# Performance work log

Measured on AMD Instinct MI355X. Metric: run time of the kernel, lower is better.

The kernel has to match this reference:

```python
import jax, jax.numpy as jnp
import numpy as np

N0 = 100000; E0 = 1600000; N1 = 100000; E1 = 1600000; G = 512
F0 = 93; F1 = 43
BN_EPS = 1e-5


def setup_inputs() -> dict:
    key = jax.random.key(0)
    ks = jax.random.split(key, 20)
    p = lambda i, shape: jax.random.normal(ks[i], shape, jnp.float32) * 0.02
    return {
        "x_0": jax.random.normal(ks[0], (N0, F0), jnp.float32),
        "x_1": jax.random.normal(ks[1], (N1, F1), jnp.float32),
        "edge_index_0": jax.random.randint(ks[2], (2, E0), 0, N0, jnp.int32),
        "edge_index_1": jax.random.randint(ks[3], (2, E1), 0, N1, jnp.int32),
        "batch_0": jnp.sort(jax.random.randint(ks[4], (N0,), 0, G, jnp.int32)),
        "batch_1": jnp.sort(jax.random.randint(ks[5], (N1,), 0, G, jnp.int32)),
        "w_c1": p(6, (F0, F0)), "b_c1": jnp.zeros((F0,), jnp.float32),
        "w_c2": p(7, (F0, F0 * 10)), "b_c2": jnp.zeros((F0 * 10,), jnp.float32),
        "w_c3": p(8, (F1, F1)), "b_c3": jnp.zeros((F1,), jnp.float32),
        "w_c4": p(9, (F1, F1 * 10)), "b_c4": jnp.zeros((F1 * 10,), jnp.float32),
        "g0_w1": p(10, (F0 * 10 * 2, 1024)), "g0_b1": jnp.zeros((1024,), jnp.float32),
        "g0_w2": p(11, (1024, 512)), "g0_b2": jnp.zeros((512,), jnp.float32),
        "g0_bn_g": jnp.ones((512,), jnp.float32), "g0_bn_b": jnp.zeros((512,), jnp.float32),
        "g1_w1": p(12, (F1 * 10 * 2, 1024)), "g1_b1": jnp.zeros((1024,), jnp.float32),
        "g1_w2": p(13, (1024, 512)), "g1_b2": jnp.zeros((512,), jnp.float32),
        "g1_bn_g": jnp.ones((512,), jnp.float32), "g1_bn_b": jnp.zeros((512,), jnp.float32),
        "f0_w1": p(14, (512, 256)), "f0_b1": jnp.zeros((256,), jnp.float32),
        "f0_w2": p(15, (256, 2)), "f0_b2": jnp.zeros((2,), jnp.float32),
        "f1_w1": p(16, (512, 256)), "f1_b1": jnp.zeros((256,), jnp.float32),
        "f1_w2": p(17, (256, 2)), "f1_b2": jnp.zeros((2,), jnp.float32),
    }


def gin_conv(x, edge_index, W, b):
    # GINConv(eps=0): nn(x + sum_{j->i} x_j); messages from src=edge_index[0] to dst=edge_index[1]
    agg = jax.ops.segment_sum(x[edge_index[0]], edge_index[1], num_segments=x.shape[0])
    return (x + agg) @ W + b


def pool_mean_max(x, batch):
    cnt = jax.ops.segment_sum(jnp.ones((x.shape[0], 1), x.dtype), batch, num_segments=G)
    mean = jax.ops.segment_sum(x, batch, num_segments=G) / jnp.maximum(cnt, 1.0)
    mx = jax.ops.segment_max(x, batch, num_segments=G)
    mx = jnp.where(cnt > 0, mx, 0.0)
    return jnp.concatenate([mean, mx], axis=1)


def batchnorm(x, g, b):
    m = x.mean(axis=0)
    v = x.var(axis=0)
    return g * (x - m) / jnp.sqrt(v + BN_EPS) + b


def branch(x, ei, batch, w_a, b_a, w_b, b_b, w1, b1, w2, b2, bn_g, bn_b):
    h = jax.nn.relu(gin_conv(x, ei, w_a, b_a))
    h = jax.nn.relu(gin_conv(h, ei, w_b, b_b))
    h = pool_mean_max(h, batch)              # [G, 2*10*F] ; PairNorm(mode='None') is identity
    h = jax.nn.relu(h @ w1 + b1)             # dropout: eval mode (identity)
    h = h @ w2 + b2
    return batchnorm(h, bn_g, bn_b)          # [G, 512]


def reference(x_0, x_1, edge_index_0, edge_index_1, batch_0, batch_1,
              w_c1, b_c1, w_c2, b_c2, w_c3, b_c3, w_c4, b_c4,
              g0_w1, g0_b1, g0_w2, g0_b2, g0_bn_g, g0_bn_b,
              g1_w1, g1_b1, g1_w2, g1_b2, g1_bn_g, g1_bn_b,
              f0_w1, f0_b1, f0_w2, f0_b2, f1_w1, f1_b1, f1_w2, f1_b2):
    x_g_0 = branch(x_0, edge_index_0, batch_0, w_c1, b_c1, w_c2, b_c2,
                   g0_w1, g0_b1, g0_w2, g0_b2, g0_bn_g, g0_bn_b)
    z = jax.nn.relu(x_g_0 @ f0_w1 + f0_b1) @ f0_w2 + f0_b2
    x_g_1 = branch(x_1, edge_index_1, batch_1, w_c3, b_c3, w_c4, b_c4,
                   g1_w1, g1_b1, g1_w2, g1_b2, g1_bn_g, g1_bn_b)
    z1 = jax.nn.relu(x_g_1 @ f1_w1 + f1_b1) @ f1_w2 + f1_b2
    return (z, x_g_0, x_g_1, z1)
```

## Files before the change

kernel.cpp:

```cpp
#include <hip/hip_runtime.h>
#include <hip/hip_bf16.h>

#define N0 100000
#define E0C 1600000
#define N1 100000
#define E1C 1600000
#define GCONST 512
#define F0C 93
#define F1C 43
#define OC0 (F0C * 10)
#define OC1 (F1C * 10)
#define BN_EPS 1e-5f
#define NBKT 391

typedef __attribute__((ext_vector_type(8))) short short8;
typedef __attribute__((ext_vector_type(4))) float floatx4;

static __device__ __forceinline__ unsigned short f2bf(float f) {
    unsigned u = __float_as_uint(f);
    unsigned r = (u + 0x7FFF + ((u >> 16) & 1)) >> 16;
    return (unsigned short)r;
}
static __device__ __forceinline__ float bf2f(unsigned short u) {
    return __uint_as_float(((unsigned)u) << 16);
}
static __device__ __forceinline__ void split_bf(float v, unsigned short& h, unsigned short& l) {
    h = f2bf(v);
    l = f2bf(v - bf2f(h));
}

__global__ __launch_bounds__(256) void zero_int_kernel(int* __restrict__ p, int n) {
    int i = blockIdx.x * 256 + threadIdx.x;
    if (i < n) p[i] = 0;
}

__global__ __launch_bounds__(256) void find_starts2_kernel(const int* __restrict__ bat0,
                                                           const int* __restrict__ bat1,
                                                           int N, int G,
                                                           int* __restrict__ st0,
                                                           int* __restrict__ st1) {
    const int* batch = blockIdx.y ? bat1 : bat0;
    int* starts = blockIdx.y ? st1 : st0;
    int g = blockIdx.x * 256 + threadIdx.x;
    if (g > G) return;
    if (g == G) { starts[G] = N; return; }
    int lo = 0, hi = N;
    while (lo < hi) {
        int mid = (lo + hi) >> 1;
        if (batch[mid] < g) lo = mid + 1; else hi = mid;
    }
    starts[g] = lo;
}

__global__ __launch_bounds__(256) void bucket_count_kernel(const int* __restrict__ ei,
                                                           int E, int* __restrict__ btot) {
    __shared__ int h[NBKT];
    int t = threadIdx.x;
    for (int i = t; i < NBKT; i += 256) h[i] = 0;
    __syncthreads();
    int base = blockIdx.x * 2048;
#pragma unroll
    for (int i = 0; i < 8; ++i) {
        int e = base + i * 256 + t;
        if (e < E) atomicAdd(&h[ei[E + e] >> 8], 1);
    }
    __syncthreads();
    for (int i = t; i < NBKT; i += 256) {
        int c = h[i];
        if (c) atomicAdd(&btot[i], c);
    }
}

__global__ __launch_bounds__(512) void bucket_scan_kernel(const int* __restrict__ btot,
                                                          int* __restrict__ bbase,
                                                          int* __restrict__ bcur) {
    __shared__ int sh[512];
    int t = threadIdx.x;
    int v = (t < NBKT) ? btot[t] : 0;
    sh[t] = v;
    __syncthreads();
    for (int o = 1; o < 512; o <<= 1) {
        int add = (t >= o) ? sh[t - o] : 0;
        __syncthreads();
        sh[t] += add;
        __syncthreads();
    }
    if (t < NBKT) {
        int ex = sh[t] - v;
        bbase[t] = ex;
        bcur[t] = ex;
    }
    if (t == NBKT) bbase[t] = sh[NBKT - 1];
}

__global__ __launch_bounds__(256) void edge_bucket_kernel(const int* __restrict__ ei,
                                                          int E,
                                                          int* __restrict__ bcur,
                                                          int2* __restrict__ staging) {
    __shared__ int hist[NBKT];
    __shared__ int gbase[NBKT];
    int t = threadIdx.x;
    for (int i = t; i < NBKT; i += 256) hist[i] = 0;
    __syncthreads();
    int base = blockIdx.x * 2048;
    int srcv[8], dstv[8];
#pragma unroll
    for (int i = 0; i < 8; ++i) {
        int e = base + i * 256 + t;
        if (e < E) { srcv[i] = ei[e]; dstv[i] = ei[E + e]; }
        else dstv[i] = -1;
    }
#pragma unroll
    for (int i = 0; i < 8; ++i)
        if (dstv[i] >= 0) atomicAdd(&hist[dstv[i] >> 8], 1);
    __syncthreads();
    for (int i = t; i < NBKT; i += 256) {
        int c = hist[i];
        gbase[i] = c ? atomicAdd(&bcur[i], c) : 0;
        hist[i] = 0;
    }
    __syncthreads();
#pragma unroll
    for (int i = 0; i < 8; ++i) {
        if (dstv[i] >= 0) {
            int b = dstv[i] >> 8;
            int lofs = atomicAdd(&hist[b], 1);
            staging[gbase[b] + lofs] = make_int2(srcv[i], dstv[i]);
        }
    }
}

__global__ __launch_bounds__(256) void csr_build_kernel(const int2* __restrict__ staging,
                                                        const int* __restrict__ bbase,
                                                        int N,
                                                        int* __restrict__ rowptr,
                                                        int* __restrict__ col) {
    __shared__ int h[256];
    __shared__ int sc[256];
    int b = blockIdx.x;
    int t = threadIdx.x;
    int s = bbase[b], e = bbase[b + 1];
    h[t] = 0;
    __syncthreads();
    for (int i = s + t; i < e; i += 256)
        atomicAdd(&h[staging[i].y & 255], 1);
    __syncthreads();
    int v = h[t];
    sc[t] = v;
    __syncthreads();
    for (int o = 1; o < 256; o <<= 1) {
        int add = (t >= o) ? sc[t - o] : 0;
        __syncthreads();
        sc[t] += add;
        __syncthreads();
    }
    int ex = s + (sc[t] - v);
    int node = (b << 8) + t;
    if (node <= N) rowptr[node] = ex;
    __syncthreads();
    sc[t] = ex;
    __syncthreads();
    for (int i = s + t; i < e; i += 256) {
        int2 ed = staging[i];
        int pos = atomicAdd(&sc[ed.y & 255], 1);
        col[pos] = ed.x;
    }
}

__global__ __launch_bounds__(128) void wt_prep4_kernel(const float* __restrict__ W0,
                                                       const float* __restrict__ W1,
                                                       const float* __restrict__ W2,
                                                       const float* __restrict__ W3,
                                                       unsigned short* __restrict__ T0,
                                                       unsigned short* __restrict__ T1,
                                                       unsigned short* __restrict__ T2,
                                                       unsigned short* __restrict__ T3) {
    const float* W; unsigned short* T; int OCr, Fr, KP, RB;
    switch (blockIdx.y) {
        case 0:  W = W0; T = T0; OCr = 93;  Fr = 93; KP = 96; RB = 96;   break;
        case 1:  W = W1; T = T1; OCr = 930; Fr = 93; KP = 96; RB = 1024; break;
        case 2:  W = W2; T = T2; OCr = 43;  Fr = 43; KP = 64; RB = 48;   break;
        default: W = W3; T = T3; OCr = 430; Fr = 43; KP = 64; RB = 512;  break;
    }
    int c = blockIdx.x, k = threadIdx.x;
    if (c >= RB || k >= KP) return;
    unsigned short v = 0;
    if (c < OCr && k < Fr) v = f2bf(W[(size_t)k * OCr + c]);
    T[(size_t)c * KP + k] = v;
}

__global__ __launch_bounds__(256) void wsplit_t_kernel(const float* __restrict__ W,
                                                       unsigned short* __restrict__ Th,
                                                       unsigned short* __restrict__ Tl,
                                                       int K, int N, int KP) {
    __shared__ float tile[32][33];
    int tx = threadIdx.x & 31, ty = threadIdx.x >> 5;
    int k0 = blockIdx.x * 32, c0 = blockIdx.y * 32;
    for (int r = ty; r < 32; r += 8) {
        int k = k0 + r;
        tile[r][tx] = (k < K) ? W[(size_t)k * N + c0 + tx] : 0.f;
    }
    __syncthreads();
    for (int r = ty; r < 32; r += 8) {
        int c = c0 + r;
        float v = tile[tx][r];
        unsigned short h, l;
        split_bf(v, h, l);
        Th[(size_t)c * KP + k0 + tx] = h;
        Tl[(size_t)c * KP + k0 + tx] = l;
    }
}

__global__ __launch_bounds__(256) void zero_pad_kernel(unsigned short* __restrict__ ph,
                                                       unsigned short* __restrict__ pl,
                                                       int KP, int from) {
    int padw = KP - from;
    int total = GCONST * padw;
    int i = blockIdx.x * 256 + threadIdx.x;
    if (i >= total) return;
    int g = i / padw, c = from + (i - g * padw);
    ph[(size_t)g * KP + c] = 0;
    pl[(size_t)g * KP + c] = 0;
}

template<int F, int KP>
__global__ __launch_bounds__(256) void tobf16_kernel(unsigned short* __restrict__ t,
                                                     const float* __restrict__ x, int N) {
    int node = blockIdx.x * blockDim.y + threadIdx.y;
    int f = threadIdx.x;
    if (node >= N) return;
    t[(size_t)node * KP + f] = (f < F) ? f2bf(x[(size_t)node * F + f]) : (unsigned short)0;
}

template<int KP, int CH, int GR>
__global__ __launch_bounds__(256) void gather_wave_kernel(unsigned short* __restrict__ t,
                                                          const unsigned short* __restrict__ x,
                                                          const int* __restrict__ rowptr,
                                                          const int* __restrict__ col,
                                                          int N) {
    int wave = threadIdx.x >> 6, lane = threadIdx.x & 63;
    int node = blockIdx.x * 4 + wave;
    if (node >= N) return;
    int g = lane / CH;
    int c = lane - g * CH;
    bool act = (g < GR);
    int s = rowptr[node], e = rowptr[node + 1];
    float acc[8] = {0.f, 0.f, 0.f, 0.f, 0.f, 0.f, 0.f, 0.f};
    int j = act ? (s - 1 + g) : e;
    int src = node;
    if (j >= s && j < e) src = col[j];
    while (j < e) {
        int jn = j + GR;
        int srcn = (jn < e) ? col[jn] : 0;
        short8 v = *(const short8*)(x + (size_t)src * KP + c * 8);
#pragma unroll
        for (int i = 0; i < 8; ++i) acc[i] += bf2f((unsigned short)v[i]);
        j = jn; src = srcn;
    }
    if (GR == 8) {
#pragma unroll
        for (int i = 0; i < 8; ++i) {
            float v = acc[i];
            v += __shfl_xor(v, 8);
            v += __shfl_xor(v, 16);
            v += __shfl_xor(v, 32);
            acc[i] = v;
        }
    } else {
#pragma unroll
        for (int i = 0; i < 8; ++i) {
            float v = acc[i];
            float v1 = __shfl(v, lane + CH);
            float v2 = __shfl(v, lane + 2 * CH);
            float v3 = __shfl(v, lane + 3 * CH);
            float v4 = __shfl(v, lane + 4 * CH);
            acc[i] = v + v1 + v2 + v3 + v4;
        }
    }
    if (lane < CH) {
        short8 o;
#pragma unroll
        for (int i = 0; i < 8; ++i) o[i] = (short)f2bf(acc[i]);
        *(short8*)(t + (size_t)node * KP + lane * 8) = o;
    }
}

template<int KP, int KS, int NT>
__global__ __launch_bounds__(256) void conv1_mfma_kernel(const unsigned short* __restrict__ t,
                                                         const unsigned short* __restrict__ Wt,
                                                         const float* __restrict__ bias,
                                                         unsigned short* __restrict__ y,
                                                         int NC, int N) {
    int wave = threadIdx.x >> 6, lane = threadIdx.x & 63;
    int quad = lane >> 4, l15 = lane & 15;
    int r0 = (blockIdx.x * 4 + wave) * 16;
    const short8 z8 = {0, 0, 0, 0, 0, 0, 0, 0};
    short8 a[KS];
    int arow = r0 + l15;
#pragma unroll
    for (int ks = 0; ks < KS; ++ks)
        a[ks] = (arow < N) ? *(const short8*)(t + (size_t)arow * KP + ks * 32 + quad * 8) : z8;
#pragma unroll
    for (int nt = 0; nt < NT; ++nt) {
        int colb = nt * 16 + l15;
        floatx4 c = {0.f, 0.f, 0.f, 0.f};
#pragma unroll
        for (int ks = 0; ks < KS; ++ks) {
            short8 b = *(const short8*)(Wt + (size_t)colb * KP + ks * 32 + quad * 8);
            c = __builtin_amdgcn_mfma_f32_16x16x32_bf16(a[ks], b, c, 0, 0, 0);
        }
        float bc = (colb < NC) ? bias[colb] : 0.f;
#pragma unroll
        for (int r = 0; r < 4; ++r) {
            int row = r0 + quad * 4 + r;
            if (row < N) {
                float o = fmaxf(c[r] + bc, 0.f);
                y[(size_t)row * KP + colb] = f2bf(o);
            }
        }
    }
}

template<int KP, int KS>
__global__ __launch_bounds__(256) void conv2_pool_mfma_kernel(const unsigned short* __restrict__ t,
                                                              const unsigned short* __restrict__ Wt,
                                                              const float* __restrict__ bias,
                                                              const int* __restrict__ starts,
                                                              unsigned short* __restrict__ ph,
                                                              unsigned short* __restrict__ pl,
                                                              int OC, int KPad) {
    int wave = threadIdx.x >> 6, lane = threadIdx.x & 63;
    int quad = lane >> 4, l15 = lane & 15;
    int g = blockIdx.y;
    int cw0 = blockIdx.x * 256 + wave * 64;
    short8 bfr[4][KS];
    float bs[4];
#pragma unroll
    for (int ti = 0; ti < 4; ++ti) {
        int colb = cw0 + ti * 16 + l15;
#pragma unroll
        for (int ks = 0; ks < KS; ++ks)
            bfr[ti][ks] = *(const short8*)(Wt + (size_t)colb * KP + ks * 32 + quad * 8);
        bs[ti] = (colb < OC) ? bias[colb] : 0.f;
    }
    int s = starts[g], e = starts[g + 1];
    float sum[4] = {0.f, 0.f, 0.f, 0.f};
    float mx[4]  = {0.f, 0.f, 0.f, 0.f};
    const short8 z8 = {0, 0, 0, 0, 0, 0, 0, 0};
    for (int ns = s; ns < e; ns += 16) {
        short8 a[KS];
        int arow = ns + l15;
        bool av = arow < e;
#pragma unroll
        for (int ks = 0; ks < KS; ++ks)
            a[ks] = av ? *(const short8*)(t + (size_t)arow * KP + ks * 32 + quad * 8) : z8;
        int rbase = ns + quad * 4;
#pragma unroll
        for (int ti = 0; ti < 4; ++ti) {
            floatx4 c = {0.f, 0.f, 0.f, 0.f};
#pragma unroll
            for (int ks = 0; ks < KS; ++ks)
                c = __builtin_amdgcn_mfma_f32_16x16x32_bf16(a[ks], bfr[ti][ks], c, 0, 0, 0);
#pragma unroll
            for (int r = 0; r < 4; ++r) {
                float o = fmaxf(c[r] + bs[ti], 0.f);
                if (rbase + r < e) {
                    sum[ti] += o;
                    mx[ti] = fmaxf(mx[ti], o);
                }
            }
        }
    }
    int cnt = e - s;
    float rc = 1.f / (float)(cnt > 0 ? cnt : 1);
#pragma unroll
    for (int ti = 0; ti < 4; ++ti) {
        float sv = sum[ti], mv = mx[ti];
        sv += __shfl_down(sv, 32);
        mv = fmaxf(mv, __shfl_down(mv, 32));
        sv += __shfl_down(sv, 16);
        mv = fmaxf(mv, __shfl_down(mv, 16));
        if (lane < 16) {
            int colb = cw0 + ti * 16 + l15;
            if (colb < OC) {
                size_t base = (size_t)g * (size_t)KPad;
                unsigned short h, l;
                split_bf(sv * rc, h, l);
                ph[base + colb] = h; pl[base + colb] = l;
                split_bf(mv, h, l);
                ph[base + OC + colb] = h; pl[base + OC + colb] = l;
            }
        }
    }
}

template<int MODE>
__global__ __launch_bounds__(256) void gemm3x_kernel(const unsigned short* __restrict__ Ah,
                                                     const unsigned short* __restrict__ Al,
                                                     const unsigned short* __restrict__ Bh,
                                                     const unsigned short* __restrict__ Bl,
                                                     const float* __restrict__ bias,
                                                     float* __restrict__ Cf,
                                                     unsigned short* __restrict__ Ch,
                                                     unsigned short* __restrict__ Cl,
                                                     int KP) {
    int wave = threadIdx.x >> 6, lane = threadIdx.x & 63;
    int quad = lane >> 4, l15 = lane & 15;
    int r0 = blockIdx.y * 32 + (wave & 1) * 16;
    int c0 = blockIdx.x * 64 + (wave >> 1) * 32;
    int Ncols = gridDim.x * 64;
    floatx4 acc0 = {0.f, 0.f, 0.f, 0.f};
    floatx4 acc1 = {0.f, 0.f, 0.f, 0.f};
    const unsigned short* arh = Ah + (size_t)(r0 + l15) * KP;
    const unsigned short* arl = Al + (size_t)(r0 + l15) * KP;
    const unsigned short* b0h = Bh + (size_t)(c0 + l15) * KP;
    const unsigned short* b0l = Bl + (size_t)(c0 + l15) * KP;
    const unsigned short* b1h = Bh + (size_t)(c0 + 16 + l15) * KP;
    const unsigned short* b1l = Bl + (size_t)(c0 + 16 + l15) * KP;
    for (int k0 = 0; k0 < KP; k0 += 128) {
        short8 ah[4], al[4];
#pragma unroll
        for (int q = 0; q < 4; ++q) {
            ah[q] = *(const short8*)(arh + k0 + q * 32 + quad * 8);
            al[q] = *(const short8*)(arl + k0 + q * 32 + quad * 8);
        }
#pragma unroll
        for (int q = 0; q < 4; ++q) {
            short8 bh = *(const short8*)(b0h + k0 + q * 32 + quad * 8);
            short8 bl = *(const short8*)(b0l + k0 + q * 32 + quad * 8);
            acc0 = __builtin_amdgcn_mfma_f32_16x16x32_bf16(ah[q], bh, acc0, 0, 0, 0);
            acc0 = __builtin_amdgcn_mfma_f32_16x16x32_bf16(al[q], bh, acc0, 0, 0, 0);
            acc0 = __builtin_amdgcn_mfma_f32_16x16x32_bf16(ah[q], bl, acc0, 0, 0, 0);
            bh = *(const short8*)(b1h + k0 + q * 32 + quad * 8);
            bl = *(const short8*)(b1l + k0 + q * 32 + quad * 8);
            acc1 = __builtin_amdgcn_mfma_f32_16x16x32_bf16(ah[q], bh, acc1, 0, 0, 0);
            acc1 = __builtin_amdgcn_mfma_f32_16x16x32_bf16(al[q], bh, acc1, 0, 0, 0);
            acc1 = __builtin_amdgcn_mfma_f32_16x16x32_bf16(ah[q], bl, acc1, 0, 0, 0);
        }
    }
    int col0 = c0 + l15, col1 = c0 + 16 + l15;
    float bc0 = bias[col0], bc1 = bias[col1];
#pragma unroll
    for (int r = 0; r < 4; ++r) {
        int row = r0 + quad * 4 + r;
        float v0 = acc0[r] + bc0;
        float v1 = acc1[r] + bc1;
        if (MODE != 1) { v0 = fmaxf(v0, 0.f); v1 = fmaxf(v1, 0.f); }
        if (MODE == 0) {
            unsigned short h, l;
            split_bf(v0, h, l);
            Ch[(size_t)row * Ncols + col0] = h; Cl[(size_t)row * Ncols + col0] = l;
            split_bf(v1, h, l);
            Ch[(size_t)row * Ncols + col1] = h; Cl[(size_t)row * Ncols + col1] = l;
        } else {
            Cf[(size_t)row * Ncols + col0] = v0;
            Cf[(size_t)row * Ncols + col1] = v1;
        }
    }
}

__global__ __launch_bounds__(256) void head2_kernel(const float* __restrict__ h,
                                                    const float* __restrict__ w2,
                                                    const float* __restrict__ b2,
                                                    float* __restrict__ z, int M) {
    int wave = threadIdx.x >> 6, lane = threadIdx.x & 63;
    int row = blockIdx.x * 4 + wave;
    if (row >= M) return;
    float4 hv = *(const float4*)(h + (size_t)row * 256 + lane * 4);
    const float* wp = w2 + lane * 8;
    float s0 = hv.x * wp[0] + hv.y * wp[2] + hv.z * wp[4] + hv.w * wp[6];
    float s1 = hv.x * wp[1] + hv.y * wp[3] + hv.z * wp[5] + hv.w * wp[7];
#pragma unroll
    for (int offd = 32; offd >= 1; offd >>= 1) {
        s0 += __shfl_down(s0, offd);
        s1 += __shfl_down(s1, offd);
    }
    if (lane == 0) {
        z[(size_t)row * 2 + 0] = s0 + b2[0];
        z[(size_t)row * 2 + 1] = s1 + b2[1];
    }
}

__global__ __launch_bounds__(256) void bn_stats_kernel(const float* __restrict__ p,
                                                       int rows, int cols,
                                                       float* __restrict__ mean,
                                                       float* __restrict__ inv) {
    int c = blockIdx.x;
    float s = 0.f, s2 = 0.f;
    for (int r = threadIdx.x; r < rows; r += 256) {
        float v = p[(size_t)r * cols + c];
        s += v;
        s2 += v * v;
    }
    __shared__ float ls[256], ls2[256];
    ls[threadIdx.x] = s;
    ls2[threadIdx.x] = s2;
    __syncthreads();
    for (int st = 128; st > 0; st >>= 1) {
        if (threadIdx.x < st) {
            ls[threadIdx.x] += ls[threadIdx.x + st];
            ls2[threadIdx.x] += ls2[threadIdx.x + st];
        }
        __syncthreads();
    }
    if (threadIdx.x == 0) {
        float m = ls[0] / (float)rows;
        float var = ls2[0] / (float)rows - m * m;
        mean[c] = m;
        inv[c] = 1.f / sqrtf(var + BN_EPS);
    }
}

__global__ __launch_bounds__(256) void bn_apply_kernel(const float* __restrict__ p,
                                                       const float* __restrict__ gamma,
                                                       const float* __restrict__ beta,
                                                       const float* __restrict__ mean,
                                                       const float* __restrict__ inv,
                                                       float* __restrict__ outp,
                                                       unsigned short* __restrict__ oh,
                                                       unsigned short* __restrict__ ol,
                                                       int total, int cols) {
    int i = blockIdx.x * 256 + threadIdx.x;
    if (i >= total) return;
    int c = i & (cols - 1);
    float v = gamma[c] * (p[i] - mean[c]) * inv[c] + beta[c];
    outp[i] = v;
    unsigned short h, l;
    split_bf(v, h, l);
    oh[i] = h;
    ol[i] = l;
}

static inline int ceildiv(int a, int b) { return (a + b - 1) / b; }

extern "C" void kernel_launch(void* const* d_in, const int* in_sizes, int n_in,
                              void* d_out, int out_size, void* d_ws, size_t ws_size,
                              hipStream_t stream) {
    const float* x0   = (const float*)d_in[0];
    const float* x1   = (const float*)d_in[1];
    const int*   ei0  = (const int*)d_in[2];
    const int*   ei1  = (const int*)d_in[3];
    const int*   bat0 = (const int*)d_in[4];
    const int*   bat1 = (const int*)d_in[5];
    const float* w_c1 = (const float*)d_in[6];
    const float* b_c1 = (const float*)d_in[7];
    const float* w_c2 = (const float*)d_in[8];
    const float* b_c2 = (const float*)d_in[9];
    const float* w_c3 = (const float*)d_in[10];
    const float* b_c3 = (const float*)d_in[11];
    const float* w_c4 = (const float*)d_in[12];
    const float* b_c4 = (const float*)d_in[13];
    const float* g0_w1 = (const float*)d_in[14];
    const float* g0_b1 = (const float*)d_in[15];
    const float* g0_w2 = (const float*)d_in[16];
    const float* g0_b2 = (const float*)d_in[17];
    const float* g0_bn_g = (const float*)d_in[18];
    const float* g0_bn_b = (const float*)d_in[19];
    const float* g1_w1 = (const float*)d_in[20];
    const float* g1_b1 = (const float*)d_in[21];
    const float* g1_w2 = (const float*)d_in[22];
    const float* g1_b2 = (const float*)d_in[23];
    const float* g1_bn_g = (const float*)d_in[24];
    const float* g1_bn_b = (const float*)d_in[25];
    const float* f0_w1 = (const float*)d_in[26];
    const float* f0_b1 = (const float*)d_in[27];
    const float* f0_w2 = (const float*)d_in[28];
    const float* f0_b2 = (const float*)d_in[29];
    const float* f1_w1 = (const float*)d_in[30];
    const float* f1_b1 = (const float*)d_in[31];
    const float* f1_w2 = (const float*)d_in[32];
    const float* f1_b2 = (const float*)d_in[33];

    float* out = (float*)d_out;
    float* out_z   = out;
    float* out_xg0 = out + 1024;
    float* out_xg1 = out + 1024 + 262144;
    float* out_z1  = out + 1024 + 262144 + 262144;

    float* ws = (float*)d_ws;
    size_t off = 0;
    auto alloc = [&](size_t n) { float* p = ws + off; off += n; return p; };
    unsigned short* t_bf = (unsigned short*)alloc((size_t)N0 * 96 / 2);
    unsigned short* y_bf = (unsigned short*)alloc((size_t)N0 * 96 / 2);
    unsigned short* wt_a0 = (unsigned short*)alloc(96 * 96 / 2);
    unsigned short* wt_b0 = (unsigned short*)alloc(1024 * 96 / 2);
    unsigned short* wt_a1 = (unsigned short*)alloc(48 * 64 / 2);
    unsigned short* wt_b1 = (unsigned short*)alloc(512 * 64 / 2);
    unsigned short* bt1h = (unsigned short*)alloc((size_t)1024 * 1920 / 2);
    unsigned short* bt1l = (unsigned short*)alloc((size_t)1024 * 1920 / 2);
    unsigned short* bt2h = (unsigned short*)alloc((size_t)512 * 1024 / 2);
    unsigned short* bt2l = (unsigned short*)alloc((size_t)512 * 1024 / 2);
    unsigned short* bt3h = (unsigned short*)alloc((size_t)256 * 512 / 2);
    unsigned short* bt3l = (unsigned short*)alloc((size_t)256 * 512 / 2);
    unsigned short* m1h  = (unsigned short*)alloc((size_t)512 * 1024 / 2);
    unsigned short* m1l  = (unsigned short*)alloc((size_t)512 * 1024 / 2);
    unsigned short* xgh  = (unsigned short*)alloc((size_t)512 * 512 / 2);
    unsigned short* xgl  = (unsigned short*)alloc((size_t)512 * 512 / 2);
    int*   btot  = (int*)alloc(512);
    int*   bbase = (int*)alloc(512);
    int*   bcur  = (int*)alloc(512);
    size_t csr_floats = (size_t)(N0 + 4) + E0C + 2 * (size_t)E0C;
    float* regionC = alloc(csr_floats);
    int* rowptr  = (int*)regionC;
    int* colb    = rowptr + (N0 + 4);
    int2* staging = (int2*)(colb + E0C);
    float* meanb   = alloc(512);
    float* invb    = alloc(512);
    int*   starts0 = (int*)alloc(520);
    int*   starts1 = (int*)alloc(520);

    const int G = GCONST;

    find_starts2_kernel<<<dim3(3, 2), 256, 0, stream>>>(bat0, bat1, N0, G, starts0, starts1);
    wt_prep4_kernel<<<dim3(1024, 4), 128, 0, stream>>>(w_c1, w_c2, w_c3, w_c4,
                                                       wt_a0, wt_b0, wt_a1, wt_b1);

    {
        const int N = N0, E = E0C, OC = OC0;
        const int KP1 = 1920;
        unsigned short* p_hi = (unsigned short*)regionC;
        unsigned short* p_lo = p_hi + (size_t)G * KP1;
        float* pbn  = (float*)(p_hi + (size_t)G * KP1 * 2);
        float* hbuf = pbn + (size_t)G * 512;
        zero_int_kernel<<<2, 256, 0, stream>>>(btot, NBKT);
        bucket_count_kernel<<<ceildiv(E, 2048), 256, 0, stream>>>(ei0, E, btot);
        bucket_scan_kernel<<<1, 512, 0, stream>>>(btot, bbase, bcur);
        edge_bucket_kernel<<<ceildiv(E, 2048), 256, 0, stream>>>(ei0, E, bcur, staging);
        csr_build_kernel<<<NBKT, 256, 0, stream>>>(staging, bbase, N, rowptr, colb);
        tobf16_kernel<93, 96><<<ceildiv(N, 2), dim3(96, 2), 0, stream>>>(y_bf, x0, N);
        gather_wave_kernel<96, 12, 5><<<ceildiv(N, 4), 256, 0, stream>>>(
            t_bf, y_bf, rowptr, colb, N);
        conv1_mfma_kernel<96, 3, 6><<<ceildiv(N, 64), 256, 0, stream>>>(
            t_bf, wt_a0, b_c1, y_bf, 93, N);
        gather_wave_kernel<96, 12, 5><<<ceildiv(N, 4), 256, 0, stream>>>(
            t_bf, y_bf, rowptr, colb, N);
        conv2_pool_mfma_kernel<96, 3><<<dim3(4, G), 256, 0, stream>>>(
            t_bf, wt_b0, b_c2, starts0, p_hi, p_lo, OC, KP1);
        zero_pad_kernel<<<ceildiv(G * (KP1 - 2 * OC), 256), 256, 0, stream>>>(
            p_hi, p_lo, KP1, 2 * OC);
        wsplit_t_kernel<<<dim3(KP1 / 32, 1024 / 32), 256, 0, stream>>>(g0_w1, bt1h, bt1l, 2 * OC, 1024, KP1);
        wsplit_t_kernel<<<dim3(1024 / 32, 512 / 32), 256, 0, stream>>>(g0_w2, bt2h, bt2l, 1024, 512, 1024);
        wsplit_t_kernel<<<dim3(512 / 32, 256 / 32), 256, 0, stream>>>(f0_w1, bt3h, bt3l, 512, 256, 512);
        gemm3x_kernel<0><<<dim3(16, 16), 256, 0, stream>>>(
            p_hi, p_lo, bt1h, bt1l, g0_b1, nullptr, m1h, m1l, KP1);
        gemm3x_kernel<1><<<dim3(8, 16), 256, 0, stream>>>(
            m1h, m1l, bt2h, bt2l, g0_b2, pbn, nullptr, nullptr, 1024);
        bn_stats_kernel<<<512, 256, 0, stream>>>(pbn, G, 512, meanb, invb);
        bn_apply_kernel<<<ceildiv(G * 512, 256), 256, 0, stream>>>(
            pbn, g0_bn_g, g0_bn_b, meanb, invb, out_xg0, xgh, xgl, G * 512, 512);
        gemm3x_kernel<2><<<dim3(4, 16), 256, 0, stream>>>(
            xgh, xgl, bt3h, bt3l, f0_b1, hbuf, nullptr, nullptr, 512);
        head2_kernel<<<G / 4, 256, 0, stream>>>(hbuf, f0_w2, f0_b2, out_z, G);
    }

    {
        const int N = N1, E = E1C, OC = OC1;
        const int KP1 = 896;
        unsigned short* p_hi = (unsigned short*)regionC;
        unsigned short* p_lo = p_hi + (size_t)G * KP1;
        float* pbn  = (float*)(p_hi + (size_t)G * KP1 * 2);
        float* hbuf = pbn + (size_t)G * 512;
        zero_int_kernel<<<2, 256, 0, stream>>>(btot, NBKT);
        bucket_count_kernel<<<ceildiv(E, 2048), 256, 0, stream>>>(ei1, E, btot);
        bucket_scan_kernel<<<1, 512, 0, stream>>>(btot, bbase, bcur);
        edge_bucket_kernel<<<ceildiv(E, 2048), 256, 0, stream>>>(ei1, E, bcur, staging);
        csr_build_kernel<<<NBKT, 256, 0, stream>>>(staging, bbase, N, rowptr, colb);
        tobf16_kernel<43, 64><<<ceildiv(N, 4), dim3(64, 4), 0, stream>>>(y_bf, x1, N);
        gather_wave_kernel<64, 8, 8><<<ceildiv(N, 4), 256, 0, stream>>>(
            t_bf, y_bf, rowptr, colb, N);
        conv1_mfma_kernel<64, 2, 3><<<ceildiv(N, 64), 256, 0, stream>>>(
            t_bf, wt_a1, b_c3, y_bf, 43, N);
        gather_wave_kernel<64, 8, 8><<<ceildiv(N, 4), 256, 0, stream>>>(
            t_bf, y_bf, rowptr, colb, N);
        conv2_pool_mfma_kernel<64, 2><<<dim3(2, G), 256, 0, stream>>>(
            t_bf, wt_b1, b_c4, starts1, p_hi, p_lo, OC, KP1);
        zero_pad_kernel<<<ceildiv(G * (KP1 - 2 * OC), 256), 256, 0, stream>>>(
            p_hi, p_lo, KP1, 2 * OC);
        wsplit_t_kernel<<<dim3(KP1 / 32, 1024 / 32), 256, 0, stream>>>(g1_w1, bt1h, bt1l, 2 * OC, 1024, KP1);
        wsplit_t_kernel<<<dim3(1024 / 32, 512 / 32), 256, 0, stream>>>(g1_w2, bt2h, bt2l, 1024, 512, 1024);
        wsplit_t_kernel<<<dim3(512 / 32, 256 / 32), 256, 0, stream>>>(f1_w1, bt3h, bt3l, 512, 256, 512);
        gemm3x_kernel<0><<<dim3(16, 16), 256, 0, stream>>>(
            p_hi, p_lo, bt1h, bt1l, g1_b1, nullptr, m1h, m1l, KP1);
        gemm3x_kernel<1><<<dim3(8, 16), 256, 0, stream>>>(
            m1h, m1l, bt2h, bt2l, g1_b2, pbn, nullptr, nullptr, 1024);
        bn_stats_kernel<<<512, 256, 0, stream>>>(pbn, G, 512, meanb, invb);
        bn_apply_kernel<<<ceildiv(G * 512, 256), 256, 0, stream>>>(
            pbn, g1_bn_g, g1_bn_b, meanb, invb, out_xg1, xgh, xgl, G * 512, 512);
        gemm3x_kernel<2><<<dim3(4, 16), 256, 0, stream>>>(
            xgh, xgl, bt3h, bt3l, f1_b1, hbuf, nullptr, nullptr, 512);
        head2_kernel<<<G / 4, 256, 0, stream>>>(hbuf, f1_w2, f1_b2, out_z1, G);
    }
}
```

Baseline: 813.0 us.

## Interleave both GNN branches in combined fused kernels to overlap stages

Builds both edge CSRs together with blockIdx.y-batched kernels and does all six weight splits in one launch. The per-stage kernels become device functions, so each launch runs branch 0's stage k next to branch 1's stage k-1 through block-range dispatch. It also fuses BN stats and apply into one per-column block and unrolls the gather loop by two. This cuts launch count and fills the GPU during small GEMM and BN stages, at the cost of separate buffers for each branch, more memory, and heterogeneous blocks inside one launch.

```diff
diff --git a/kernel.cpp b/kernel.cpp
--- a/kernel.cpp
+++ b/kernel.cpp
@@ -52,8 +52,23 @@
     starts[g] = lo;
 }
 
-__global__ __launch_bounds__(256) void bucket_count_kernel(const int* __restrict__ ei,
-                                                           int E, int* __restrict__ btot) {
+__global__ __launch_bounds__(256) void zero_pad_kernel(unsigned short* __restrict__ ph,
+                                                       unsigned short* __restrict__ pl,
+                                                       int KP, int from) {
+    int padw = KP - from;
+    int total = GCONST * padw;
+    int i = blockIdx.x * 256 + threadIdx.x;
+    if (i >= total) return;
+    int g = i / padw, c = from + (i - g * padw);
+    ph[(size_t)g * KP + c] = 0;
+    pl[(size_t)g * KP + c] = 0;
+}
+
+__global__ __launch_bounds__(256) void bucket_count2_kernel(const int* __restrict__ ei0,
+                                                            const int* __restrict__ ei1,
+                                                            int E, int* __restrict__ btot2) {
+    const int* ei = blockIdx.y ? ei1 : ei0;
+    int* btot = btot2 + blockIdx.y * 512;
     __shared__ int h[NBKT];
     int t = threadIdx.x;
     for (int i = t; i < NBKT; i += 256) h[i] = 0;
@@ -71,9 +86,12 @@
     }
 }
 
-__global__ __launch_bounds__(512) void bucket_scan_kernel(const int* __restrict__ btot,
-                                                          int* __restrict__ bbase,
-                                                          int* __restrict__ bcur) {
+__global__ __launch_bounds__(512) void bucket_scan2_kernel(const int* __restrict__ btot2,
+                                                           int* __restrict__ bbase2,
+                                                           int* __restrict__ bcur2) {
+    const int* btot = btot2 + blockIdx.x * 512;
+    int* bbase = bbase2 + blockIdx.x * 512;
+    int* bcur  = bcur2 + blockIdx.x * 512;
     __shared__ int sh[512];
     int t = threadIdx.x;
     int v = (t < NBKT) ? btot[t] : 0;
@@ -93,10 +111,14 @@
     if (t == NBKT) bbase[t] = sh[NBKT - 1];
 }
 
-__global__ __launch_bounds__(256) void edge_bucket_kernel(const int* __restrict__ ei,
-                                                          int E,
-                                                          int* __restrict__ bcur,
-                                                          int2* __restrict__ staging) {
+__global__ __launch_bounds__(256) void edge_bucket2_kernel(const int* __restrict__ ei0,
+                                                           const int* __restrict__ ei1,
+                                                           int E, int* __restrict__ bcur2,
+                                                           int2* __restrict__ st0,
+                                                           int2* __restrict__ st1) {
+    const int* ei = blockIdx.y ? ei1 : ei0;
+    int* bcur = bcur2 + blockIdx.y * 512;
+    int2* staging = blockIdx.y ? st1 : st0;
     __shared__ int hist[NBKT];
     __shared__ int gbase[NBKT];
     int t = threadIdx.x;
@@ -130,11 +152,18 @@
     }
 }
 
-__global__ __launch_bounds__(256) void csr_build_kernel(const int2* __restrict__ staging,
-                                                        const int* __restrict__ bbase,
-                                                        int N,
-                                                        int* __restrict__ rowptr,
-                                                        int* __restrict__ col) {
+__global__ __launch_bounds__(256) void csr_build2_kernel(const int2* __restrict__ st0,
+                                                         const int2* __restrict__ st1,
+                                                         const int* __restrict__ bbase2,
+                                                         int N,
+                                                         int* __restrict__ rp0,
+                                                         int* __restrict__ rp1,
+                                                         int* __restrict__ c0,
+                                                         int* __restrict__ c1) {
+    const int2* staging = blockIdx.y ? st1 : st0;
+    const int* bbase = bbase2 + blockIdx.y * 512;
+    int* rowptr = blockIdx.y ? rp1 : rp0;
+    int* col = blockIdx.y ? c1 : c0;
     __shared__ int h[256];
     __shared__ int sc[256];
     int b = blockIdx.x;
@@ -189,13 +218,25 @@
     T[(size_t)c * KP + k] = v;
 }
 
-__global__ __launch_bounds__(256) void wsplit_t_kernel(const float* __restrict__ W,
-                                                       unsigned short* __restrict__ Th,
-                                                       unsigned short* __restrict__ Tl,
-                                                       int K, int N, int KP) {
+struct WsArgs {
+    const float* W[6];
+    unsigned short* H[6];
+    unsigned short* L[6];
+    int K[6];
+    int N[6];
+    int KP[6];
+};
+
+__global__ __launch_bounds__(256) void wsplit_all_kernel(WsArgs a) {
+    int z = blockIdx.z;
+    int K = a.K[z], N = a.N[z], KP = a.KP[z];
+    int k0 = blockIdx.x * 32, c0 = blockIdx.y * 32;
+    if (k0 >= KP || c0 >= N) return;
+    const float* W = a.W[z];
+    unsigned short* Th = a.H[z];
+    unsigned short* Tl = a.L[z];
     __shared__ float tile[32][33];
     int tx = threadIdx.x & 31, ty = threadIdx.x >> 5;
-    int k0 = blockIdx.x * 32, c0 = blockIdx.y * 32;
     for (int r = ty; r < 32; r += 8) {
         int k = k0 + r;
         tile[r][tx] = (k < K) ? W[(size_t)k * N + c0 + tx] : 0.f;
@@ -211,18 +252,6 @@
     }
 }
 
-__global__ __launch_bounds__(256) void zero_pad_kernel(unsigned short* __restrict__ ph,
-                                                       unsigned short* __restrict__ pl,
-                                                       int KP, int from) {
-    int padw = KP - from;
-    int total = GCONST * padw;
-    int i = blockIdx.x * 256 + threadIdx.x;
-    if (i >= total) return;
-    int g = i / padw, c = from + (i - g * padw);
-    ph[(size_t)g * KP + c] = 0;
-    pl[(size_t)g * KP + c] = 0;
-}
-
 template<int F, int KP>
 __global__ __launch_bounds__(256) void tobf16_kernel(unsigned short* __restrict__ t,
                                                      const float* __restrict__ x, int N) {
@@ -232,14 +261,14 @@
     t[(size_t)node * KP + f] = (f < F) ? f2bf(x[(size_t)node * F + f]) : (unsigned short)0;
 }
 
+
 template<int KP, int CH, int GR>
-__global__ __launch_bounds__(256) void gather_wave_kernel(unsigned short* __restrict__ t,
-                                                          const unsigned short* __restrict__ x,
-                                                          const int* __restrict__ rowptr,
-                                                          const int* __restrict__ col,
-                                                          int N) {
+static __device__ __forceinline__ void gather_dev(int nb, unsigned short* __restrict__ t,
+                                                  const unsigned short* __restrict__ x,
+                                                  const int* __restrict__ rowptr,
+                                                  const int* __restrict__ col, int N) {
     int wave = threadIdx.x >> 6, lane = threadIdx.x & 63;
-    int node = blockIdx.x * 4 + wave;
+    int node = nb * 4 + wave;
     if (node >= N) return;
     int g = lane / CH;
     int c = lane - g * CH;
@@ -247,15 +276,22 @@
     int s = rowptr[node], e = rowptr[node + 1];
     float acc[8] = {0.f, 0.f, 0.f, 0.f, 0.f, 0.f, 0.f, 0.f};
     int j = act ? (s - 1 + g) : e;
-    int src = node;
-    if (j >= s && j < e) src = col[j];
+    int src0 = node;
+    if (j >= s && j < e) src0 = col[j];
     while (j < e) {
-        int jn = j + GR;
-        int srcn = (jn < e) ? col[jn] : 0;
-        short8 v = *(const short8*)(x + (size_t)src * KP + c * 8);
-#pragma unroll
-        for (int i = 0; i < 8; ++i) acc[i] += bf2f((unsigned short)v[i]);
-        j = jn; src = srcn;
+        int jb = j + GR;
+        int jc = jb + GR;
+        int srcb = (jb < e) ? col[jb] : 0;
+        int srcc = (jc < e) ? col[jc] : 0;
+        short8 v0 = *(const short8*)(x + (size_t)src0 * KP + c * 8);
+#pragma unroll
+        for (int i = 0; i < 8; ++i) acc[i] += bf2f((unsigned short)v0[i]);
+        if (jb < e) {
+            short8 v1 = *(const short8*)(x + (size_t)srcb * KP + c * 8);
+#pragma unroll
+            for (int i = 0; i < 8; ++i) acc[i] += bf2f((unsigned short)v1[i]);
+        }
+        j = jc; src0 = srcc;
     }
     if (GR == 8) {
 #pragma unroll
@@ -286,14 +322,14 @@
 }
 
 template<int KP, int KS, int NT>
-__global__ __launch_bounds__(256) void conv1_mfma_kernel(const unsigned short* __restrict__ t,
-                                                         const unsigned short* __restrict__ Wt,
-                                                         const float* __restrict__ bias,
-                                                         unsigned short* __restrict__ y,
-                                                         int NC, int N) {
+static __device__ __forceinline__ void conv1_dev(int nb, const unsigned short* __restrict__ t,
+                                                 const unsigned short* __restrict__ Wt,
+                                                 const float* __restrict__ bias,
+                                                 unsigned short* __restrict__ y,
+                                                 int NC, int N) {
     int wave = threadIdx.x >> 6, lane = threadIdx.x & 63;
     int quad = lane >> 4, l15 = lane & 15;
-    int r0 = (blockIdx.x * 4 + wave) * 16;
+    int r0 = (nb * 4 + wave) * 16;
     const short8 z8 = {0, 0, 0, 0, 0, 0, 0, 0};
     short8 a[KS];
     int arow = r0 + l15;
@@ -322,17 +358,17 @@
 }
 
 template<int KP, int KS>
-__global__ __launch_bounds__(256) void conv2_pool_mfma_kernel(const unsigned short* __restrict__ t,
-                                                              const unsigned short* __restrict__ Wt,
-                                                              const float* __restrict__ bias,
-                                                              const int* __restrict__ starts,
-                                                              unsigned short* __restrict__ ph,
-                                                              unsigned short* __restrict__ pl,
-                                                              int OC, int KPad) {
+static __device__ __forceinline__ void conv2_pool_dev(int cb, int g,
+                                                      const unsigned short* __restrict__ t,
+                                                      const unsigned short* __restrict__ Wt,
+                                                      const float* __restrict__ bias,
+                                                      const int* __restrict__ starts,
+                                                      unsigned short* __restrict__ ph,
+                                                      unsigned short* __restrict__ pl,
+                                                      int OC, int KPad) {
     int wave = threadIdx.x >> 6, lane = threadIdx.x & 63;
     int quad = lane >> 4, l15 = lane & 15;
-    int g = blockIdx.y;
-    int cw0 = blockIdx.x * 256 + wave * 64;
+    int cw0 = cb * 256 + wave * 64;
     short8 bfr[4][KS];
     float bs[4];
 #pragma unroll
@@ -395,20 +431,21 @@
 }
 
 template<int MODE>
-__global__ __launch_bounds__(256) void gemm3x_kernel(const unsigned short* __restrict__ Ah,
-                                                     const unsigned short* __restrict__ Al,
-                                                     const unsigned short* __restrict__ Bh,
-                                                     const unsigned short* __restrict__ Bl,
-                                                     const float* __restrict__ bias,
-                                                     float* __restrict__ Cf,
-                                                     unsigned short* __restrict__ Ch,
-                                                     unsigned short* __restrict__ Cl,
-                                                     int KP) {
+static __device__ __forceinline__ void gemm3x_dev(int bx, int by, int NBX,
+                                                  const unsigned short* __restrict__ Ah,
+                                                  const unsigned short* __restrict__ Al,
+                                                  const unsigned short* __restrict__ Bh,
+                                                  const unsigned short* __restrict__ Bl,
+                                                  const float* __restrict__ bias,
+                                                  float* __restrict__ Cf,
+                                                  unsigned short* __restrict__ Ch,
+                                                  unsigned short* __restrict__ Cl,
+                                                  int KP) {
     int wave = threadIdx.x >> 6, lane = threadIdx.x & 63;
     int quad = lane >> 4, l15 = lane & 15;
-    int r0 = blockIdx.y * 32 + (wave & 1) * 16;
-    int c0 = blockIdx.x * 64 + (wave >> 1) * 32;
-    int Ncols = gridDim.x * 64;
+    int r0 = by * 32 + (wave & 1) * 16;
+    int c0 = bx * 64 + (wave >> 1) * 32;
+    int Ncols = NBX * 64;
     floatx4 acc0 = {0.f, 0.f, 0.f, 0.f};
     floatx4 acc1 = {0.f, 0.f, 0.f, 0.f};
     const unsigned short* arh = Ah + (size_t)(r0 + l15) * KP;
@@ -459,12 +496,49 @@
     }
 }
 
-__global__ __launch_bounds__(256) void head2_kernel(const float* __restrict__ h,
-                                                    const float* __restrict__ w2,
-                                                    const float* __restrict__ b2,
-                                                    float* __restrict__ z, int M) {
+static __device__ __forceinline__ void bn_dev(int c, const float* __restrict__ p,
+                                              const float* __restrict__ gamma,
+                                              const float* __restrict__ beta,
+                                              float* __restrict__ outp,
+                                              unsigned short* __restrict__ oh,
+                                              unsigned short* __restrict__ ol) {
+    __shared__ float ls[256], ls2[256];
+    int t = threadIdx.x;
+    float v0 = p[(size_t)t * 512 + c];
+    float v1 = p[(size_t)(t + 256) * 512 + c];
+    ls[t] = v0 + v1;
+    ls2[t] = v0 * v0 + v1 * v1;
+    __syncthreads();
+    for (int st = 128; st > 0; st >>= 1) {
+        if (t < st) { ls[t] += ls[t + st]; ls2[t] += ls2[t + st]; }
+        __syncthreads();
+    }
+    if (t == 0) {
+        float m = ls[0] / 512.f;
+        float var = ls2[0] / 512.f - m * m;
+        ls[0] = m;
+        ls2[0] = 1.f / sqrtf(var + BN_EPS);
+    }
+    __syncthreads();
+    float m = ls[0], iv = ls2[0];
+    float g = gamma[c], b = beta[c];
+    float w0 = g * (v0 - m) * iv + b;
+    float w1 = g * (v1 - m) * iv + b;
+    outp[(size_t)t * 512 + c] = w0;
+    outp[(size_t)(t + 256) * 512 + c] = w1;
+    unsigned short h, l;
+    split_bf(w0, h, l);
+    oh[(size_t)t * 512 + c] = h; ol[(size_t)t * 512 + c] = l;
+    split_bf(w1, h, l);
+    oh[(size_t)(t + 256) * 512 + c] = h; ol[(size_t)(t + 256) * 512 + c] = l;
+}
+
+static __device__ __forceinline__ void head2_dev(int nb, const float* __restrict__ h,
+                                                 const float* __restrict__ w2,
+                                                 const float* __restrict__ b2,
+                                                 float* __restrict__ z, int M) {
     int wave = threadIdx.x >> 6, lane = threadIdx.x & 63;
-    int row = blockIdx.x * 4 + wave;
+    int row = nb * 4 + wave;
     if (row >= M) return;
     float4 hv = *(const float4*)(h + (size_t)row * 256 + lane * 4);
     const float* wp = w2 + lane * 8;
@@ -481,54 +555,134 @@
     }
 }
 
-__global__ __launch_bounds__(256) void bn_stats_kernel(const float* __restrict__ p,
-                                                       int rows, int cols,
-                                                       float* __restrict__ mean,
-                                                       float* __restrict__ inv) {
-    int c = blockIdx.x;
-    float s = 0.f, s2 = 0.f;
-    for (int r = threadIdx.x; r < rows; r += 256) {
-        float v = p[(size_t)r * cols + c];
-        s += v;
-        s2 += v * v;
-    }
-    __shared__ float ls[256], ls2[256];
-    ls[threadIdx.x] = s;
-    ls2[threadIdx.x] = s2;
-    __syncthreads();
-    for (int st = 128; st > 0; st >>= 1) {
-        if (threadIdx.x < st) {
-            ls[threadIdx.x] += ls[threadIdx.x + st];
-            ls2[threadIdx.x] += ls2[threadIdx.x + st];
-        }
-        __syncthreads();
-    }
-    if (threadIdx.x == 0) {
-        float m = ls[0] / (float)rows;
-        float var = ls2[0] / (float)rows - m * m;
-        mean[c] = m;
-        inv[c] = 1.f / sqrtf(var + BN_EPS);
-    }
-}
-
-__global__ __launch_bounds__(256) void bn_apply_kernel(const float* __restrict__ p,
-                                                       const float* __restrict__ gamma,
-                                                       const float* __restrict__ beta,
-                                                       const float* __restrict__ mean,
-                                                       const float* __restrict__ inv,
-                                                       float* __restrict__ outp,
-                                                       unsigned short* __restrict__ oh,
-                                                       unsigned short* __restrict__ ol,
-                                                       int total, int cols) {
-    int i = blockIdx.x * 256 + threadIdx.x;
-    if (i >= total) return;
-    int c = i & (cols - 1);
-    float v = gamma[c] * (p[i] - mean[c]) * inv[c] + beta[c];
-    outp[i] = v;
-    unsigned short h, l;
-    split_bf(v, h, l);
-    oh[i] = h;
-    ol[i] = l;
+template<int KP, int CH, int GR>
+__global__ __launch_bounds__(256) void gather_wave_kernel(unsigned short* __restrict__ t,
+                                                          const unsigned short* __restrict__ x,
+                                                          const int* __restrict__ rowptr,
+                                                          const int* __restrict__ col, int N) {
+    gather_dev<KP, CH, GR>(blockIdx.x, t, x, rowptr, col, N);
+}
+
+__global__ __launch_bounds__(256) void head2_kernel(const float* __restrict__ h,
+                                                    const float* __restrict__ w2,
+                                                    const float* __restrict__ b2,
+                                                    float* __restrict__ z, int M) {
+    head2_dev(blockIdx.x, h, w2, b2, z, M);
+}
+
+__global__ __launch_bounds__(256) void f2_kernel(
+        const unsigned short* tb, const unsigned short* wt_a0, const float* b_c1,
+        unsigned short* yb,
+        unsigned short* t1, const unsigned short* xb1,
+        const int* rowptr1, const int* col1) {
+    int bid = blockIdx.x;
+    if (bid < 1563)
+        conv1_dev<96, 3, 6>(bid, tb, wt_a0, b_c1, yb, 93, N0);
+    else
+        gather_dev<64, 8, 8>(bid - 1563, t1, xb1, rowptr1, col1, N1);
+}
+
+__global__ __launch_bounds__(256) void f3_kernel(
+        unsigned short* tb, const unsigned short* yb,
+        const int* rowptr0, const int* col0,
+        const unsigned short* t1, const unsigned short* wt_a1, const float* b_c3,
+        unsigned short* y1) {
+    int bid = blockIdx.x;
+    if (bid < 25000)
+        gather_dev<96, 12, 5>(bid, tb, yb, rowptr0, col0, N0);
+    else
+        conv1_dev<64, 2, 3>(bid - 25000, t1, wt_a1, b_c3, y1, 43, N1);
+}
+
+__global__ __launch_bounds__(256) void f4_kernel(
+        const unsigned short* tb, const unsigned short* wt_b0, const float* b_c2,
+        const int* starts0, unsigned short* p0h, unsigned short* p0l,
+        unsigned short* t1, const unsigned short* y1,
+        const int* rowptr1, const int* col1) {
+    int bid = blockIdx.x;
+    if (bid < 2048)
+        conv2_pool_dev<96, 3>(bid & 3, bid >> 2, tb, wt_b0, b_c2, starts0, p0h, p0l, OC0, 1920);
+    else
+        gather_dev<64, 8, 8>(bid - 2048, t1, y1, rowptr1, col1, N1);
+}
+
+__global__ __launch_bounds__(256) void f5_kernel(
+        const unsigned short* p0h, const unsigned short* p0l,
+        const unsigned short* bt1h0, const unsigned short* bt1l0, const float* g0_b1,
+        unsigned short* m1h0, unsigned short* m1l0,
+        const unsigned short* t1, const unsigned short* wt_b1, const float* b_c4,
+        const int* starts1, unsigned short* p1h, unsigned short* p1l) {
+    int bid = blockIdx.x;
+    if (bid < 256)
+        gemm3x_dev<0>(bid & 15, bid >> 4, 16, p0h, p0l, bt1h0, bt1l0, g0_b1,
+                      nullptr, m1h0, m1l0, 1920);
+    else {
+        int b = bid - 256;
+        conv2_pool_dev<64, 2>(b & 1, b >> 1, t1, wt_b1, b_c4, starts1, p1h, p1l, OC1, 896);
+    }
+}
+
+__global__ __launch_bounds__(256) void f6_kernel(
+        const unsigned short* m1h0, const unsigned short* m1l0,
+        const unsigned short* bt2h0, const unsigned short* bt2l0, const float* g0_b2,
+        float* pbn0,
+        const unsigned short* p1h, const unsigned short* p1l,
+        const unsigned short* bt1h1, const unsigned short* bt1l1, const float* g1_b1,
+        unsigned short* m1h1, unsigned short* m1l1) {
+    int bid = blockIdx.x;
+    if (bid < 128)
+        gemm3x_dev<1>(bid & 7, bid >> 3, 8, m1h0, m1l0, bt2h0, bt2l0, g0_b2,
+                      pbn0, nullptr, nullptr, 1024);
+    else {
+        int b = bid - 128;
+        gemm3x_dev<0>(b & 15, b >> 4, 16, p1h, p1l, bt1h1, bt1l1, g1_b1,
+                      nullptr, m1h1, m1l1, 896);
+    }
+}
+
+__global__ __launch_bounds__(256) void f7_kernel(
+        const float* pbn0, const float* g0_bn_g, const float* g0_bn_b,
+        float* out_xg0, unsigned short* xgh0, unsigned short* xgl0,
+        const unsigned short* m1h1, const unsigned short* m1l1,
+        const unsigned short* bt2h1, const unsigned short* bt2l1, const float* g1_b2,
+        float* pbn1) {
+    int bid = blockIdx.x;
+    if (bid < 512)
+        bn_dev(bid, pbn0, g0_bn_g, g0_bn_b, out_xg0, xgh0, xgl0);
+    else {
+        int b = bid - 512;
+        gemm3x_dev<1>(b & 7, b >> 3, 8, m1h1, m1l1, bt2h1, bt2l1, g1_b2,
+                      pbn1, nullptr, nullptr, 1024);
+    }
+}
+
+__global__ __launch_bounds__(256) void f8_kernel(
+        const unsigned short* xgh0, const unsigned short* xgl0,
+        const unsigned short* bt3h0, const unsigned short* bt3l0, const float* f0_b1,
+        float* hbuf0,
+        const float* pbn1, const float* g1_bn_g, const float* g1_bn_b,
+        float* out_xg1, unsigned short* xgh1, unsigned short* xgl1) {
+    int bid = blockIdx.x;
+    if (bid < 64)
+        gemm3x_dev<2>(bid & 3, bid >> 2, 4, xgh0, xgl0, bt3h0, bt3l0, f0_b1,
+                      hbuf0, nullptr, nullptr, 512);
+    else
+        bn_dev(bid - 64, pbn1, g1_bn_g, g1_bn_b, out_xg1, xgh1, xgl1);
+}
+
+__global__ __launch_bounds__(256) void f9_kernel(
+        const float* hbuf0, const float* f0_w2, const float* f0_b2, float* out_z,
+        const unsigned short* xgh1, const unsigned short* xgl1,
+        const unsigned short* bt3h1, const unsigned short* bt3l1, const float* f1_b1,
+        float* hbuf1) {
+    int bid = blockIdx.x;
+    if (bid < 128)
+        head2_dev(bid, hbuf0, f0_w2, f0_b2, out_z, GCONST);
+    else {
+        int b = bid - 128;
+        gemm3x_dev<2>(b & 3, b >> 2, 4, xgh1, xgl1, bt3h1, bt3l1, f1_b1,
+                      hbuf1, nullptr, nullptr, 512);
+    }
 }
 
 static inline int ceildiv(int a, int b) { return (a + b - 1) / b; }
@@ -580,114 +734,99 @@
     float* ws = (float*)d_ws;
     size_t off = 0;
     auto alloc = [&](size_t n) { float* p = ws + off; off += n; return p; };
-    unsigned short* t_bf = (unsigned short*)alloc((size_t)N0 * 96 / 2);
-    unsigned short* y_bf = (unsigned short*)alloc((size_t)N0 * 96 / 2);
+    unsigned short* xb0 = (unsigned short*)alloc((size_t)N0 * 96 / 2);
+    unsigned short* xb1 = (unsigned short*)alloc((size_t)N1 * 64 / 2);
+    unsigned short* tb  = (unsigned short*)alloc((size_t)N0 * 96 / 2);
+    unsigned short* yb  = (unsigned short*)alloc((size_t)N0 * 96 / 2);
     unsigned short* wt_a0 = (unsigned short*)alloc(96 * 96 / 2);
     unsigned short* wt_b0 = (unsigned short*)alloc(1024 * 96 / 2);
     unsigned short* wt_a1 = (unsigned short*)alloc(48 * 64 / 2);
     unsigned short* wt_b1 = (unsigned short*)alloc(512 * 64 / 2);
-    unsigned short* bt1h = (unsigned short*)alloc((size_t)1024 * 1920 / 2);
-    unsigned short* bt1l = (unsigned short*)alloc((size_t)1024 * 1920 / 2);
-    unsigned short* bt2h = (unsigned short*)alloc((size_t)512 * 1024 / 2);
-    unsigned short* bt2l = (unsigned short*)alloc((size_t)512 * 1024 / 2);
-    unsigned short* bt3h = (unsigned short*)alloc((size_t)256 * 512 / 2);
-    unsigned short* bt3l = (unsigned short*)alloc((size_t)256 * 512 / 2);
-    unsigned short* m1h  = (unsigned short*)alloc((size_t)512 * 1024 / 2);
-    unsigned short* m1l  = (unsigned short*)alloc((size_t)512 * 1024 / 2);
-    unsigned short* xgh  = (unsigned short*)alloc((size_t)512 * 512 / 2);
-    unsigned short* xgl  = (unsigned short*)alloc((size_t)512 * 512 / 2);
-    int*   btot  = (int*)alloc(512);
-    int*   bbase = (int*)alloc(512);
-    int*   bcur  = (int*)alloc(512);
-    size_t csr_floats = (size_t)(N0 + 4) + E0C + 2 * (size_t)E0C;
-    float* regionC = alloc(csr_floats);
-    int* rowptr  = (int*)regionC;
-    int* colb    = rowptr + (N0 + 4);
-    int2* staging = (int2*)(colb + E0C);
-    float* meanb   = alloc(512);
-    float* invb    = alloc(512);
-    int*   starts0 = (int*)alloc(520);
-    int*   starts1 = (int*)alloc(520);
+    unsigned short* bt1h0 = (unsigned short*)alloc((size_t)1024 * 1920 / 2);
+    unsigned short* bt1l0 = (unsigned short*)alloc((size_t)1024 * 1920 / 2);
+    unsigned short* bt2h0 = (unsigned short*)alloc((size_t)512 * 1024 / 2);
+    unsigned short* bt2l0 = (unsigned short*)alloc((size_t)512 * 1024 / 2);
+    unsigned short* bt3h0 = (unsigned short*)alloc((size_t)256 * 512 / 2);
+    unsigned short* bt3l0 = (unsigned short*)alloc((size_t)256 * 512 / 2);
+    unsigned short* bt1h1 = (unsigned short*)alloc((size_t)1024 * 896 / 2);
+    unsigned short* bt1l1 = (unsigned short*)alloc((size_t)1024 * 896 / 2);
+    unsigned short* bt2h1 = (unsigned short*)alloc((size_t)512 * 1024 / 2);
+    unsigned short* bt2l1 = (unsigned short*)alloc((size_t)512 * 1024 / 2);
+    unsigned short* bt3h1 = (unsigned short*)alloc((size_t)256 * 512 / 2);
+    unsigned short* bt3l1 = (unsigned short*)alloc((size_t)256 * 512 / 2);
+    unsigned short* m1h0 = (unsigned short*)alloc((size_t)512 * 1024 / 2);
+    unsigned short* m1l0 = (unsigned short*)alloc((size_t)512 * 1024 / 2);
+    unsigned short* m1h1 = (unsigned short*)alloc((size_t)512 * 1024 / 2);
+    unsigned short* m1l1 = (unsigned short*)alloc((size_t)512 * 1024 / 2);
+    unsigned short* xgh0 = (unsigned short*)alloc((size_t)512 * 512 / 2);
+    unsigned short* xgl0 = (unsigned short*)alloc((size_t)512 * 512 / 2);
+    unsigned short* xgh1 = (unsigned short*)alloc((size_t)512 * 512 / 2);
+    unsigned short* xgl1 = (unsigned short*)alloc((size_t)512 * 512 / 2);
+    unsigned short* p0h = (unsigned short*)alloc((size_t)512 * 1920 / 2);
+    unsigned short* p0l = (unsigned short*)alloc((size_t)512 * 1920 / 2);
+    unsigned short* p1h = (unsigned short*)alloc((size_t)512 * 896 / 2);
+    unsigned short* p1l = (unsigned short*)alloc((size_t)512 * 896 / 2);
+    float* pbn0  = alloc((size_t)512 * 512);
+    float* pbn1  = alloc((size_t)512 * 512);
+    float* hbuf0 = alloc((size_t)512 * 256);
+    float* hbuf1 = alloc((size_t)512 * 256);
+    int* btot2  = (int*)alloc(1024);
+    int* bbase2 = (int*)alloc(1024);
+    int* bcur2  = (int*)alloc(1024);
+    int* rowptr0 = (int*)alloc(100016);
+    int* col0    = (int*)alloc(E0C);
+    int* rowptr1 = (int*)alloc(100016);
+    int* col1    = (int*)alloc(E1C);
+    int* starts0 = (int*)alloc(520);
+    int* starts1 = (int*)alloc(520);
+    int2* staging0 = (int2*)tb;
+    int2* staging1 = (int2*)yb;
+    unsigned short* t1 = xb0;
+    unsigned short* y1 = xb1;
 
     const int G = GCONST;
+    const int EB = ceildiv(E0C, 2048);
 
     find_starts2_kernel<<<dim3(3, 2), 256, 0, stream>>>(bat0, bat1, N0, G, starts0, starts1);
     wt_prep4_kernel<<<dim3(1024, 4), 128, 0, stream>>>(w_c1, w_c2, w_c3, w_c4,
                                                        wt_a0, wt_b0, wt_a1, wt_b1);
-
     {
-        const int N = N0, E = E0C, OC = OC0;
-        const int KP1 = 1920;
-        unsigned short* p_hi = (unsigned short*)regionC;
-        unsigned short* p_lo = p_hi + (size_t)G * KP1;
-        float* pbn  = (float*)(p_hi + (size_t)G * KP1 * 2);
-        float* hbuf = pbn + (size_t)G * 512;
-        zero_int_kernel<<<2, 256, 0, stream>>>(btot, NBKT);
-        bucket_count_kernel<<<ceildiv(E, 2048), 256, 0, stream>>>(ei0, E, btot);
-        bucket_scan_kernel<<<1, 512, 0, stream>>>(btot, bbase, bcur);
-        edge_bucket_kernel<<<ceildiv(E, 2048), 256, 0, stream>>>(ei0, E, bcur, staging);
-        csr_build_kernel<<<NBKT, 256, 0, stream>>>(staging, bbase, N, rowptr, colb);
-        tobf16_kernel<93, 96><<<ceildiv(N, 2), dim3(96, 2), 0, stream>>>(y_bf, x0, N);
-        gather_wave_kernel<96, 12, 5><<<ceildiv(N, 4), 256, 0, stream>>>(
-            t_bf, y_bf, rowptr, colb, N);
-        conv1_mfma_kernel<96, 3, 6><<<ceildiv(N, 64), 256, 0, stream>>>(
-            t_bf, wt_a0, b_c1, y_bf, 93, N);
-        gather_wave_kernel<96, 12, 5><<<ceildiv(N, 4), 256, 0, stream>>>(
-            t_bf, y_bf, rowptr, colb, N);
-        conv2_pool_mfma_kernel<96, 3><<<dim3(4, G), 256, 0, stream>>>(
-            t_bf, wt_b0, b_c2, starts0, p_hi, p_lo, OC, KP1);
-        zero_pad_kernel<<<ceildiv(G * (KP1 - 2 * OC), 256), 256, 0, stream>>>(
-            p_hi, p_lo, KP1, 2 * OC);
-        wsplit_t_kernel<<<dim3(KP1 / 32, 1024 / 32), 256, 0, stream>>>(g0_w1, bt1h, bt1l, 2 * OC, 1024, KP1);
-        wsplit_t_kernel<<<dim3(1024 / 32, 512 / 32), 256, 0, stream>>>(g0_w2, bt2h, bt2l, 1024, 512, 1024);
-        wsplit_t_kernel<<<dim3(512 / 32, 256 / 32), 256, 0, stream>>>(f0_w1, bt3h, bt3l, 512, 256, 512);
-        gemm3x_kernel<0><<<dim3(16, 16), 256, 0, stream>>>(
-            p_hi, p_lo, bt1h, bt1l, g0_b1, nullptr, m1h, m1l, KP1);
-        gemm3x_kernel<1><<<dim3(8, 16), 256, 0, stream>>>(
-            m1h, m1l, bt2h, bt2l, g0_b2, pbn, nullptr, nullptr, 1024);
-        bn_stats_kernel<<<512, 256, 0, stream>>>(pbn, G, 512, meanb, invb);
-        bn_apply_kernel<<<ceildiv(G * 512, 256), 256, 0, stream>>>(
-            pbn, g0_bn_g, g0_bn_b, meanb, invb, out_xg0, xgh, xgl, G * 512, 512);
-        gemm3x_kernel<2><<<dim3(4, 16), 256, 0, stream>>>(
-            xgh, xgl, bt3h, bt3l, f0_b1, hbuf, nullptr, nullptr, 512);
-        head2_kernel<<<G / 4, 256, 0, stream>>>(hbuf, f0_w2, f0_b2, out_z, G);
-    }
-
-    {
-        const int N = N1, E = E1C, OC = OC1;
-        const int KP1 = 896;
-        unsigned short* p_hi = (unsigned short*)regionC;
-        unsigned short* p_lo = p_hi + (size_t)G * KP1;
-        float* pbn  = (float*)(p_hi + (size_t)G * KP1 * 2);
-        float* hbuf = pbn + (size_t)G * 512;
-        zero_int_kernel<<<2, 256, 0, stream>>>(btot, NBKT);
-        bucket_count_kernel<<<ceildiv(E, 2048), 256, 0, stream>>>(ei1, E, btot);
-        bucket_scan_kernel<<<1, 512, 0, stream>>>(btot, bbase, bcur);
-        edge_bucket_kernel<<<ceildiv(E, 2048), 256, 0, stream>>>(ei1, E, bcur, staging);
-        csr_build_kernel<<<NBKT, 256, 0, stream>>>(staging, bbase, N, rowptr, colb);
-        tobf16_kernel<43, 64><<<ceildiv(N, 4), dim3(64, 4), 0, stream>>>(y_bf, x1, N);
-        gather_wave_kernel<64, 8, 8><<<ceildiv(N, 4), 256, 0, stream>>>(
-            t_bf, y_bf, rowptr, colb, N);
-        conv1_mfma_kernel<64, 2, 3><<<ceildiv(N, 64), 256, 0, stream>>>(
-            t_bf, wt_a1, b_c3, y_bf, 43, N);
-        gather_wave_kernel<64, 8, 8><<<ceildiv(N, 4), 256, 0, stream>>>(
-            t_bf, y_bf, rowptr, colb, N);
-        conv2_pool_mfma_kernel<64, 2><<<dim3(2, G), 256, 0, stream>>>(
-            t_bf, wt_b1, b_c4, starts1, p_hi, p_lo, OC, KP1);
-        zero_pad_kernel<<<ceildiv(G * (KP1 - 2 * OC), 256), 256, 0, stream>>>(
-            p_hi, p_lo, KP1, 2 * OC);
-        wsplit_t_kernel<<<dim3(KP1 / 32, 1024 / 32), 256, 0, stream>>>(g1_w1, bt1h, bt1l, 2 * OC, 1024, KP1);
-        wsplit_t_kernel<<<dim3(1024 / 32, 512 / 32), 256, 0, stream>>>(g1_w2, bt2h, bt2l, 1024, 512, 1024);
-        wsplit_t_kernel<<<dim3(512 / 32, 256 / 32), 256, 0, stream>>>(f1_w1, bt3h, bt3l, 512, 256, 512);
-        gemm3x_kernel<0><<<dim3(16, 16), 256, 0, stream>>>(
-            p_hi, p_lo, bt1h, bt1l, g1_b1, nullptr, m1h, m1l, KP1);
-        gemm3x_kernel<1><<<dim3(8, 16), 256, 0, stream>>>(
-            m1h, m1l, bt2h, bt2l, g1_b2, pbn, nullptr, nullptr, 1024);
-        bn_stats_kernel<<<512, 256, 0, stream>>>(pbn, G, 512, meanb, invb);
-        bn_apply_kernel<<<ceildiv(G * 512, 256), 256, 0, stream>>>(
-            pbn, g1_bn_g, g1_bn_b, meanb, invb, out_xg1, xgh, xgl, G * 512, 512);
-        gemm3x_kernel<2><<<dim3(4, 16), 256, 0, stream>>>(
-            xgh, xgl, bt3h, bt3l, f1_b1, hbuf, nullptr, nullptr, 512);
-        head2_kernel<<<G / 4, 256, 0, stream>>>(hbuf, f1_w2, f1_b2, out_z1, G);
-    }
-}
+        WsArgs a;
+        a.W[0] = g0_w1; a.H[0] = bt1h0; a.L[0] = bt1l0; a.K[0] = 1860; a.N[0] = 1024; a.KP[0] = 1920;
+        a.W[1] = g0_w2; a.H[1] = bt2h0; a.L[1] = bt2l0; a.K[1] = 1024; a.N[1] = 512;  a.KP[1] = 1024;
+        a.W[2] = f0_w1; a.H[2] = bt3h0; a.L[2] = bt3l0; a.K[2] = 512;  a.N[2] = 256;  a.KP[2] = 512;
+        a.W[3] = g1_w1; a.H[3] = bt1h1; a.L[3] = bt1l1; a.K[3] = 860;  a.N[3] = 1024; a.KP[3] = 896;
+        a.W[4] = g1_w2; a.H[4] = bt2h1; a.L[4] = bt2l1; a.K[4] = 1024; a.N[4] = 512;  a.KP[4] = 1024;
+        a.W[5] = f1_w1; a.H[5] = bt3h1; a.L[5] = bt3l1; a.K[5] = 512;  a.N[5] = 256;  a.KP[5] = 512;
+        wsplit_all_kernel<<<dim3(60, 32, 6), 256, 0, stream>>>(a);
+    }
+    zero_pad_kernel<<<ceildiv(G * (1920 - 2 * OC0), 256), 256, 0, stream>>>(p0h, p0l, 1920, 2 * OC0);
+    zero_pad_kernel<<<ceildiv(G * (896 - 2 * OC1), 256), 256, 0, stream>>>(p1h, p1l, 896, 2 * OC1);
+    zero_int_kernel<<<4, 256, 0, stream>>>(btot2, 1024);
+    bucket_count2_kernel<<<dim3(EB, 2), 256, 0, stream>>>(ei0, ei1, E0C, btot2);
+    bucket_scan2_kernel<<<2, 512, 0, stream>>>(btot2, bbase2, bcur2);
+    edge_bucket2_kernel<<<dim3(EB, 2), 256, 0, stream>>>(ei0, ei1, E0C, bcur2, staging0, staging1);
+    csr_build2_kernel<<<dim3(NBKT, 2), 256, 0, stream>>>(staging0, staging1, bbase2, N0,
+                                                         rowptr0, rowptr1, col0, col1);
+    tobf16_kernel<93, 96><<<ceildiv(N0, 2), dim3(96, 2), 0, stream>>>(xb0, x0, N0);
+    tobf16_kernel<43, 64><<<ceildiv(N1, 4), dim3(64, 4), 0, stream>>>(xb1, x1, N1);
+
+    gather_wave_kernel<96, 12, 5><<<25000, 256, 0, stream>>>(tb, xb0, rowptr0, col0, N0);
+    f2_kernel<<<1563 + 25000, 256, 0, stream>>>(tb, wt_a0, b_c1, yb,
+                                                t1, xb1, rowptr1, col1);
+    f3_kernel<<<25000 + 1563, 256, 0, stream>>>(tb, yb, rowptr0, col0,
+                                                t1, wt_a1, b_c3, y1);
+    f4_kernel<<<2048 + 25000, 256, 0, stream>>>(tb, wt_b0, b_c2, starts0, p0h, p0l,
+                                                t1, y1, rowptr1, col1);
+    f5_kernel<<<256 + 1024, 256, 0, stream>>>(p0h, p0l, bt1h0, bt1l0, g0_b1, m1h0, m1l0,
+                                              t1, wt_b1, b_c4, starts1, p1h, p1l);
+    f6_kernel<<<128 + 256, 256, 0, stream>>>(m1h0, m1l0, bt2h0, bt2l0, g0_b2, pbn0,
+                                             p1h, p1l, bt1h1, bt1l1, g1_b1, m1h1, m1l1);
+    f7_kernel<<<512 + 128, 256, 0, stream>>>(pbn0, g0_bn_g, g0_bn_b, out_xg0, xgh0, xgl0,
+                                             m1h1, m1l1, bt2h1, bt2l1, g1_b2, pbn1);
+    f8_kernel<<<64 + 512, 256, 0, stream>>>(xgh0, xgl0, bt3h0, bt3l0, f0_b1, hbuf0,
+                                            pbn1, g1_bn_g, g1_bn_b, out_xg1, xgh1, xgl1);
+    f9_kernel<<<128 + 64, 256, 0, stream>>>(hbuf0, f0_w2, f0_b2, out_z,
+                                            xgh1, xgl1, bt3h1, bt3l1, f1_b1, hbuf1);
+    head2_kernel<<<G / 4, 256, 0, stream>>>(hbuf1, f1_w2, f1_b2, out_z1, G);
+}
```

New measurement: 738.6 us. 9.2% less time.
